# Kernel optimization log

Hardware: AMD Instinct MI355X
Metric: run time of the kernel (lower is better)

The kernel has to match this reference:

```python
import jax, jax.numpy as jnp
import numpy as np

BETA = 1.0
EPS = 1e-8  # matches torch F.cosine_similarity eps


def setup_inputs() -> dict:
    key = jax.random.key(0)
    x = jax.random.normal(key, (4096, 2, 1024), dtype=jnp.float32)
    return {"x": x}


def _cosine_sim_matrix(pos, anc):
    # pos: [B, D], anc: [B, D] -> [B, B], sim[i, j] = cos(pos[i], anc[j])
    dots = jnp.einsum('id,jd->ij', pos, anc)
    pn = jnp.sqrt(jnp.sum(pos * pos, axis=-1))
    an = jnp.sqrt(jnp.sum(anc * anc, axis=-1))
    denom = jnp.maximum(pn[:, None] * an[None, :], EPS)
    return dots / denom


def reference(x):
    # x: [B, M, D], M >= 2
    out_anchor = jnp.mean(x[:, 1:, :], axis=1)   # [B, D]
    out_positive = x[:, 0, :]                     # [B, D]
    sim = _cosine_sim_matrix(out_positive, out_anchor)  # [B, B]
    n = sim.shape[0]

    diag = jnp.diagonal(sim)                      # [B]
    # tempsim for column i: beta * (sim[:, i] - sim[i, i]), excluding row i
    T = BETA * (sim - diag[None, :])              # [B, B]
    eye = jnp.eye(n, dtype=bool)

    # exclude-diagonal logsumexp per column (vectorized over all columns)
    Tm = jnp.where(eye, -jnp.inf, T)
    temploss = jax.nn.logsumexp(Tm, axis=0)       # [B]
    # flatNCE trick: exp(l - stop_grad(l)) has value 1 but gradient of l
    nloss = jnp.mean(jnp.exp(temploss - jax.lax.stop_gradient(temploss)))

    # top-1 accuracy against labels arange(B) (detached in original)
    label = jnp.arange(n)
    prec1 = jnp.mean((jnp.argmax(sim, axis=1) == label).astype(jnp.float32)) * 100.0
    return nloss, prec1
```

## Files before the change

kernel.cpp:

```cpp
#include <hip/hip_runtime.h>


#define NROWS 4096
#define DDIM  1024
#define XSTR  2048

typedef unsigned int u32;
typedef unsigned long long u64;
typedef __attribute__((ext_vector_type(8))) short bf16x8;
typedef __attribute__((ext_vector_type(16))) float f32x16;

__device__ __forceinline__ unsigned int fkey(float f) {
    unsigned int u = __float_as_uint(f);
    return (u & 0x80000000u) ? ~u : (u | 0x80000000u);
}

__device__ __forceinline__ u64 shfl_xor_u64(u64 v, int m) {
    unsigned int lo = (unsigned int)v;
    unsigned int hi = (unsigned int)(v >> 32);
    lo = __shfl_xor(lo, m, 64);
    hi = __shfl_xor(hi, m, 64);
    return ((u64)hi << 32) | lo;
}

__device__ __forceinline__ unsigned short f2bf(float f) {
    unsigned u = __float_as_uint(f);
    return (unsigned short)((u + 0x7FFFu + ((u >> 16) & 1u)) >> 16);
}

#define PF_OFF   0u
#define AF_OFF   8388608u
#define INV_OFF  16777216u
#define PCK_OFF  16793600u
#define DONE_OFF 16826368u
#define WS_NEED  16826432u

__global__ __launch_bounds__(256) void prep_kernel(const float* __restrict__ x,
                                                   unsigned short* __restrict__ Pf,
                                                   unsigned short* __restrict__ Af,
                                                   float* __restrict__ inv_an,
                                                   u64* __restrict__ packed,
                                                   unsigned int* __restrict__ done) {
    __shared__ float rsum[256];
    const int b = blockIdx.x;
    const int t = threadIdx.x;
    const int l31 = t & 31;
    const int lh = (t >> 5) & 1;
    const int row = b * 32 + l31;

    const float* px = x + (size_t)row * XSTR;
    unsigned short* pdst = Pf + (size_t)b * 32768;
    unsigned short* adst = Af + (size_t)b * 32768;

    float s = 0.0f;
#pragma unroll
    for (int i = 0; i < 16; ++i) {
        const int g = i * 256 + t;
        const int kcol = (g >> 6) * 16 + lh * 8;

        float4 p0 = *(const float4*)(px + kcol);
        float4 p1 = *(const float4*)(px + kcol + 4);
        float4 a0 = *(const float4*)(px + DDIM + kcol);
        float4 a1 = *(const float4*)(px + DDIM + kcol + 4);

        ushort4 h0 = make_ushort4(f2bf(p0.x), f2bf(p0.y), f2bf(p0.z), f2bf(p0.w));
        ushort4 h1 = make_ushort4(f2bf(p1.x), f2bf(p1.y), f2bf(p1.z), f2bf(p1.w));
        *(ushort4*)(pdst + g * 8) = h0;
        *(ushort4*)(pdst + g * 8 + 4) = h1;

        ushort4 g0 = make_ushort4(f2bf(a0.x), f2bf(a0.y), f2bf(a0.z), f2bf(a0.w));
        ushort4 g1 = make_ushort4(f2bf(a1.x), f2bf(a1.y), f2bf(a1.z), f2bf(a1.w));
        *(ushort4*)(adst + g * 8) = g0;
        *(ushort4*)(adst + g * 8 + 4) = g1;

        s += a0.x * a0.x + a0.y * a0.y + a0.z * a0.z + a0.w * a0.w;
        s += a1.x * a1.x + a1.y * a1.y + a1.z * a1.z + a1.w * a1.w;
    }
    rsum[t] = s;
    __syncthreads();
    if (t < 32) {
        float tot = 0.0f;
#pragma unroll
        for (int w = 0; w < 8; ++w) tot += rsum[t + 32 * w];
        inv_an[b * 32 + t] = 1.0f / sqrtf(tot);
        packed[b * 32 + t] = 0ULL;
        if (b == 0 && t == 0) *done = 0u;
    }
}

#define FRAG(base, blk, kh) (*(const bf16x8*)((base) + (((size_t)(blk)) << 16) + ((kh) << 10)))

__global__ __launch_bounds__(256, 1) void mfma_gemm_argmax(const unsigned short* __restrict__ Pf,
                                                           const unsigned short* __restrict__ Af,
                                                           const float* __restrict__ inv_an,
                                                           u64* __restrict__ packed,
                                                           unsigned int* __restrict__ done,
                                                           float* __restrict__ out) {
    __shared__ unsigned int lastflag;
    __shared__ int cnt[4];

    const int bid = blockIdx.x;
    const int xcd = bid & 7;
    const int slt = bid >> 3;
    const int rblk = (xcd >> 1) * 4 + (slt >> 3);
    const int cblk = (xcd & 1) * 8 + (slt & 7);
    const int r0 = rblk * 256;
    const int c0 = cblk * 256;

    const int wave = threadIdx.x >> 6;
    const int lane = threadIdx.x & 63;
    const int l31 = lane & 31;
    const int lh = lane >> 5;
    const int wm = wave & 1;
    const int wn = wave >> 1;

    const int mb0 = rblk * 8 + wm * 4;
    const int nb0 = cblk * 8 + wn * 4;

    const char* pP = (const char*)Pf + (size_t)lane * 16 + ((size_t)mb0 << 16);
    const char* pA = (const char*)Af + (size_t)lane * 16 + ((size_t)nb0 << 16);

    f32x16 zero16 = {0.f,0.f,0.f,0.f,0.f,0.f,0.f,0.f,0.f,0.f,0.f,0.f,0.f,0.f,0.f,0.f};
    f32x16 acc[4][4];
#pragma unroll
    for (int i = 0; i < 4; ++i)
#pragma unroll
        for (int j = 0; j < 4; ++j) acc[i][j] = zero16;

    bf16x8 phA[4], aaA[4], phB[4], aaB[4];

#pragma unroll
    for (int q = 0; q < 4; ++q) { phA[q] = FRAG(pP, q, 0); aaA[q] = FRAG(pA, q, 0); }

    for (int kh = 0; kh < 64; kh += 2) {
#pragma unroll
        for (int q = 0; q < 4; ++q) { phB[q] = FRAG(pP, q, kh + 1); aaB[q] = FRAG(pA, q, kh + 1); }

#pragma unroll
        for (int mt = 0; mt < 4; ++mt)
#pragma unroll
            for (int nt = 0; nt < 4; ++nt)
                acc[mt][nt] = __builtin_amdgcn_mfma_f32_32x32x16_bf16(phA[mt], aaA[nt], acc[mt][nt], 0, 0, 0);

        if (kh + 2 < 64) {
#pragma unroll
            for (int q = 0; q < 4; ++q) { phA[q] = FRAG(pP, q, kh + 2); aaA[q] = FRAG(pA, q, kh + 2); }
        }

#pragma unroll
        for (int mt = 0; mt < 4; ++mt)
#pragma unroll
            for (int nt = 0; nt < 4; ++nt)
                acc[mt][nt] = __builtin_amdgcn_mfma_f32_32x32x16_bf16(phB[mt], aaB[nt], acc[mt][nt], 0, 0, 0);
    }

    float ian[4];
#pragma unroll
    for (int nt = 0; nt < 4; ++nt) ian[nt] = inv_an[c0 + wn * 128 + nt * 32 + l31];

#pragma unroll
    for (int mt = 0; mt < 4; ++mt)
#pragma unroll
        for (int reg = 0; reg < 16; ++reg) {
            const int row = r0 + wm * 128 + mt * 32 + (reg & 3) + 8 * (reg >> 2) + 4 * lh;
            u64 best = 0ULL;
#pragma unroll
            for (int nt = 0; nt < 4; ++nt) {
                const int col = c0 + wn * 128 + nt * 32 + l31;
                const float v = acc[mt][nt][reg] * ian[nt];
                const u64 p = ((u64)fkey(v) << 32) | (unsigned int)(~col);
                best = best > p ? best : p;
            }
#pragma unroll
            for (int m = 1; m <= 16; m <<= 1) {
                const u64 o = shfl_xor_u64(best, m);
                best = best > o ? best : o;
            }
            if (l31 == 0) atomicMax(&packed[row], best);
        }

    __syncthreads();
    if (threadIdx.x == 0) {
        __threadfence();
        unsigned int old = atomicAdd(done, 1u);
        lastflag = (old == 255u) ? 1u : 0u;
    }
    __syncthreads();
    if (lastflag) {
        int c = 0;
        for (int r = threadIdx.x; r < NROWS; r += 256) {
            u64 v = atomicAdd(&packed[r], 0ULL);
            unsigned int col = ~(unsigned int)(v & 0xFFFFFFFFULL);
            c += (col == (unsigned int)r) ? 1 : 0;
        }
#pragma unroll
        for (int off = 32; off > 0; off >>= 1) c += __shfl_down(c, off, 64);
        if ((threadIdx.x & 63) == 0) cnt[threadIdx.x >> 6] = c;
        __syncthreads();
        if (threadIdx.x == 0) {
            out[0] = 1.0f;
            out[1] = 100.0f * (float)(cnt[0] + cnt[1] + cnt[2] + cnt[3]) / (float)NROWS;
        }
    }
}

__global__ __launch_bounds__(256) void norms_kernel(const float* __restrict__ x,
                                                    float* __restrict__ inv_an,
                                                    u64* __restrict__ packed) {
    int gid  = blockIdx.x * 256 + threadIdx.x;
    int j    = gid >> 6;
    int lane = threadIdx.x & 63;
    if (gid < NROWS) packed[gid] = 0ULL;
    const float4* a = (const float4*)(x + (size_t)j * XSTR + DDIM);
    float s = 0.0f;
#pragma unroll
    for (int i = 0; i < 4; ++i) {
        float4 v = a[lane + i * 64];
        s += v.x * v.x + v.y * v.y + v.z * v.z + v.w * v.w;
    }
#pragma unroll
    for (int off = 32; off > 0; off >>= 1) s += __shfl_down(s, off, 64);
    if (lane == 0) inv_an[j] = 1.0f / sqrtf(s);
}

__global__ __launch_bounds__(256) void gemm_argmax_kernel(const float* __restrict__ x,
                                                          const float* __restrict__ inv_an,
                                                          u64* __restrict__ packed) {
    __shared__ __align__(16) float Pt[16][128];
    __shared__ __align__(16) float At[16][128];
    const int r0 = blockIdx.x * 128;
    const int c0 = blockIdx.y * 128;
    const int t = threadIdx.x;
    const int tx = t & 15;
    const int ty = t >> 4;
    const int srow = t >> 1;
    const int skq = (t & 1) * 8;
    float acc[8][8];
#pragma unroll
    for (int r = 0; r < 8; ++r)
#pragma unroll
        for (int c = 0; c < 8; ++c) acc[r][c] = 0.0f;
    const float* gp = x + (size_t)(r0 + srow) * XSTR + skq;
    const float* ga = x + (size_t)(c0 + srow) * XSTR + DDIM + skq;
    for (int k0 = 0; k0 < DDIM; k0 += 16) {
        __syncthreads();
        float4 p0 = *(const float4*)(gp + k0);
        float4 p1 = *(const float4*)(gp + k0 + 4);
        float4 a0 = *(const float4*)(ga + k0);
        float4 a1 = *(const float4*)(ga + k0 + 4);
        Pt[skq + 0][srow] = p0.x; Pt[skq + 1][srow] = p0.y;
        Pt[skq + 2][srow] = p0.z; Pt[skq + 3][srow] = p0.w;
        Pt[skq + 4][srow] = p1.x; Pt[skq + 5][srow] = p1.y;
        Pt[skq + 6][srow] = p1.z; Pt[skq + 7][srow] = p1.w;
        At[skq + 0][srow] = a0.x; At[skq + 1][srow] = a0.y;
        At[skq + 2][srow] = a0.z; At[skq + 3][srow] = a0.w;
        At[skq + 4][srow] = a1.x; At[skq + 5][srow] = a1.y;
        At[skq + 6][srow] = a1.z; At[skq + 7][srow] = a1.w;
        __syncthreads();
#pragma unroll
        for (int kk = 0; kk < 16; ++kk) {
            float pr[8], ar[8];
            *(float4*)&pr[0] = *(const float4*)&Pt[kk][ty * 8];
            *(float4*)&pr[4] = *(const float4*)&Pt[kk][ty * 8 + 4];
            *(float4*)&ar[0] = *(const float4*)&At[kk][tx * 8];
            *(float4*)&ar[4] = *(const float4*)&At[kk][tx * 8 + 4];
#pragma unroll
            for (int r = 0; r < 8; ++r)
#pragma unroll
                for (int c = 0; c < 8; ++c) acc[r][c] += pr[r] * ar[c];
        }
    }
    float ian[8];
#pragma unroll
    for (int c = 0; c < 8; ++c) ian[c] = inv_an[c0 + tx * 8 + c];
#pragma unroll
    for (int r = 0; r < 8; ++r) {
        int row = r0 + ty * 8 + r;
        u64 best = 0ULL;
#pragma unroll
        for (int c = 0; c < 8; ++c) {
            int col = c0 + tx * 8 + c;
            float v = acc[r][c] * ian[c];
            u64 p = ((u64)fkey(v) << 32) | (unsigned int)(~col);
            best = best > p ? best : p;
        }
#pragma unroll
        for (int m = 1; m <= 8; m <<= 1) {
            u64 o = shfl_xor_u64(best, m);
            best = best > o ? best : o;
        }
        if (tx == 0) atomicMax(&packed[row], best);
    }
}

__global__ __launch_bounds__(256) void finalize_kernel(const u64* __restrict__ packed,
                                                       float* __restrict__ out) {
    __shared__ int cnt_s;
    int t = threadIdx.x;
    if (t == 0) cnt_s = 0;
    __syncthreads();
    int c = 0;
    for (int r = t; r < NROWS; r += 256) {
        unsigned int col = ~(unsigned int)(packed[r] & 0xFFFFFFFFULL);
        c += (col == (unsigned int)r) ? 1 : 0;
    }
#pragma unroll
    for (int off = 32; off > 0; off >>= 1) c += __shfl_down(c, off, 64);
    if ((t & 63) == 0) atomicAdd(&cnt_s, c);
    __syncthreads();
    if (t == 0) {
        out[0] = 1.0f;
        out[1] = 100.0f * (float)cnt_s / (float)NROWS;
    }
}

extern "C" void kernel_launch(void* const* d_in, const int* in_sizes, int n_in,
                              void* d_out, int out_size, void* d_ws, size_t ws_size,
                              hipStream_t stream) {
    (void)in_sizes; (void)n_in; (void)out_size;
    const float* x = (const float*)d_in[0];
    float* out = (float*)d_out;

    if (ws_size >= (size_t)WS_NEED) {
        char* ws = (char*)d_ws;
        unsigned short* Pf = (unsigned short*)(ws + PF_OFF);
        unsigned short* Af = (unsigned short*)(ws + AF_OFF);
        float* inv_an = (float*)(ws + INV_OFF);
        u64* packed = (u64*)(ws + PCK_OFF);
        unsigned int* done = (unsigned int*)(ws + DONE_OFF);

        prep_kernel<<<128, 256, 0, stream>>>(x, Pf, Af, inv_an, packed, done);
        mfma_gemm_argmax<<<256, 256, 0, stream>>>(Pf, Af, inv_an, packed, done, out);
    } else {
        float* inv_an = (float*)d_ws;
        u64* packed = (u64*)((char*)d_ws + NROWS * sizeof(float));
        norms_kernel<<<NROWS / 4, 256, 0, stream>>>(x, inv_an, packed);
        dim3 grid(NROWS / 128, NROWS / 128);
        gemm_argmax_kernel<<<grid, 256, 0, stream>>>(x, inv_an, packed);
        finalize_kernel<<<1, 256, 0, stream>>>(packed, out);
    }
}
```

Before: 131.8 us.

## Use 8 waves per GEMM block with smaller per-wave tiles and triple-buffered fragments

Doubles the GEMM block to 512 threads (8 waves), so each wave computes a 64x128 tile instead of 128x128. This halves the accumulator registers per wave and raises the number of resident waves available to hide global-load latency. The two-stage A/B fragment ping-pong becomes a fully unrolled three-stage rotating buffer that prefetches two k-steps ahead. In exchange, each wave reuses loaded fragments across fewer MFMAs, so total global and L2 fragment traffic grows, and the full unroll increases code size.

```diff
diff --git a/kernel.cpp b/kernel.cpp
--- a/kernel.cpp
+++ b/kernel.cpp
@@ -63,15 +63,10 @@
         float4 a0 = *(const float4*)(px + DDIM + kcol);
         float4 a1 = *(const float4*)(px + DDIM + kcol + 4);
 
-        ushort4 h0 = make_ushort4(f2bf(p0.x), f2bf(p0.y), f2bf(p0.z), f2bf(p0.w));
-        ushort4 h1 = make_ushort4(f2bf(p1.x), f2bf(p1.y), f2bf(p1.z), f2bf(p1.w));
-        *(ushort4*)(pdst + g * 8) = h0;
-        *(ushort4*)(pdst + g * 8 + 4) = h1;
-
-        ushort4 g0 = make_ushort4(f2bf(a0.x), f2bf(a0.y), f2bf(a0.z), f2bf(a0.w));
-        ushort4 g1 = make_ushort4(f2bf(a1.x), f2bf(a1.y), f2bf(a1.z), f2bf(a1.w));
-        *(ushort4*)(adst + g * 8) = g0;
-        *(ushort4*)(adst + g * 8 + 4) = g1;
+        *(ushort4*)(pdst + g * 8) = make_ushort4(f2bf(p0.x), f2bf(p0.y), f2bf(p0.z), f2bf(p0.w));
+        *(ushort4*)(pdst + g * 8 + 4) = make_ushort4(f2bf(p1.x), f2bf(p1.y), f2bf(p1.z), f2bf(p1.w));
+        *(ushort4*)(adst + g * 8) = make_ushort4(f2bf(a0.x), f2bf(a0.y), f2bf(a0.z), f2bf(a0.w));
+        *(ushort4*)(adst + g * 8 + 4) = make_ushort4(f2bf(a1.x), f2bf(a1.y), f2bf(a1.z), f2bf(a1.w));
 
         s += a0.x * a0.x + a0.y * a0.y + a0.z * a0.z + a0.w * a0.w;
         s += a1.x * a1.x + a1.y * a1.y + a1.z * a1.z + a1.w * a1.w;
@@ -90,14 +85,14 @@
 
 #define FRAG(base, blk, kh) (*(const bf16x8*)((base) + (((size_t)(blk)) << 16) + ((kh) << 10)))
 
-__global__ __launch_bounds__(256, 1) void mfma_gemm_argmax(const unsigned short* __restrict__ Pf,
+__global__ __launch_bounds__(512, 2) void mfma_gemm_argmax(const unsigned short* __restrict__ Pf,
                                                            const unsigned short* __restrict__ Af,
                                                            const float* __restrict__ inv_an,
                                                            u64* __restrict__ packed,
                                                            unsigned int* __restrict__ done,
                                                            float* __restrict__ out) {
     __shared__ unsigned int lastflag;
-    __shared__ int cnt[4];
+    __shared__ int cnt[8];
 
     const int bid = blockIdx.x;
     const int xcd = bid & 7;
@@ -111,47 +106,43 @@
     const int lane = threadIdx.x & 63;
     const int l31 = lane & 31;
     const int lh = lane >> 5;
-    const int wm = wave & 1;
-    const int wn = wave >> 1;
-
-    const int mb0 = rblk * 8 + wm * 4;
+    const int wm = wave & 3;
+    const int wn = wave >> 2;
+
+    const int mb0 = rblk * 8 + wm * 2;
     const int nb0 = cblk * 8 + wn * 4;
 
     const char* pP = (const char*)Pf + (size_t)lane * 16 + ((size_t)mb0 << 16);
     const char* pA = (const char*)Af + (size_t)lane * 16 + ((size_t)nb0 << 16);
 
     f32x16 zero16 = {0.f,0.f,0.f,0.f,0.f,0.f,0.f,0.f,0.f,0.f,0.f,0.f,0.f,0.f,0.f,0.f};
-    f32x16 acc[4][4];
-#pragma unroll
-    for (int i = 0; i < 4; ++i)
+    f32x16 acc[2][4];
+#pragma unroll
+    for (int i = 0; i < 2; ++i)
 #pragma unroll
         for (int j = 0; j < 4; ++j) acc[i][j] = zero16;
 
-    bf16x8 phA[4], aaA[4], phB[4], aaB[4];
-
-#pragma unroll
-    for (int q = 0; q < 4; ++q) { phA[q] = FRAG(pP, q, 0); aaA[q] = FRAG(pA, q, 0); }
-
-    for (int kh = 0; kh < 64; kh += 2) {
-#pragma unroll
-        for (int q = 0; q < 4; ++q) { phB[q] = FRAG(pP, q, kh + 1); aaB[q] = FRAG(pA, q, kh + 1); }
-
-#pragma unroll
-        for (int mt = 0; mt < 4; ++mt)
+    bf16x8 ph[3][2], aa[3][4];
+#pragma unroll
+    for (int q = 0; q < 2; ++q) { ph[0][q] = FRAG(pP, q, 0); ph[1][q] = FRAG(pP, q, 1); }
+#pragma unroll
+    for (int q = 0; q < 4; ++q) { aa[0][q] = FRAG(pA, q, 0); aa[1][q] = FRAG(pA, q, 1); }
+
+#pragma unroll
+    for (int kh = 0; kh < 64; ++kh) {
+        const int cs = kh % 3;
+        if (kh + 2 < 64) {
+            const int ns = (kh + 2) % 3;
+#pragma unroll
+            for (int q = 0; q < 2; ++q) ph[ns][q] = FRAG(pP, q, kh + 2);
+#pragma unroll
+            for (int q = 0; q < 4; ++q) aa[ns][q] = FRAG(pA, q, kh + 2);
+        }
+#pragma unroll
+        for (int mt = 0; mt < 2; ++mt)
 #pragma unroll
             for (int nt = 0; nt < 4; ++nt)
-                acc[mt][nt] = __builtin_amdgcn_mfma_f32_32x32x16_bf16(phA[mt], aaA[nt], acc[mt][nt], 0, 0, 0);
-
-        if (kh + 2 < 64) {
-#pragma unroll
-            for (int q = 0; q < 4; ++q) { phA[q] = FRAG(pP, q, kh + 2); aaA[q] = FRAG(pA, q, kh + 2); }
-        }
-
-#pragma unroll
-        for (int mt = 0; mt < 4; ++mt)
-#pragma unroll
-            for (int nt = 0; nt < 4; ++nt)
-                acc[mt][nt] = __builtin_amdgcn_mfma_f32_32x32x16_bf16(phB[mt], aaB[nt], acc[mt][nt], 0, 0, 0);
+                acc[mt][nt] = __builtin_amdgcn_mfma_f32_32x32x16_bf16(ph[cs][mt], aa[cs][nt], acc[mt][nt], 0, 0, 0);
     }
 
     float ian[4];
@@ -159,10 +150,10 @@
     for (int nt = 0; nt < 4; ++nt) ian[nt] = inv_an[c0 + wn * 128 + nt * 32 + l31];
 
 #pragma unroll
-    for (int mt = 0; mt < 4; ++mt)
+    for (int mt = 0; mt < 2; ++mt)
 #pragma unroll
         for (int reg = 0; reg < 16; ++reg) {
-            const int row = r0 + wm * 128 + mt * 32 + (reg & 3) + 8 * (reg >> 2) + 4 * lh;
+            const int row = r0 + wm * 64 + mt * 32 + (reg & 3) + 8 * (reg >> 2) + 4 * lh;
             u64 best = 0ULL;
 #pragma unroll
             for (int nt = 0; nt < 4; ++nt) {
@@ -188,7 +179,7 @@
     __syncthreads();
     if (lastflag) {
         int c = 0;
-        for (int r = threadIdx.x; r < NROWS; r += 256) {
+        for (int r = threadIdx.x; r < NROWS; r += 512) {
             u64 v = atomicAdd(&packed[r], 0ULL);
             unsigned int col = ~(unsigned int)(v & 0xFFFFFFFFULL);
             c += (col == (unsigned int)r) ? 1 : 0;
@@ -198,8 +189,11 @@
         if ((threadIdx.x & 63) == 0) cnt[threadIdx.x >> 6] = c;
         __syncthreads();
         if (threadIdx.x == 0) {
+            int tot = 0;
+#pragma unroll
+            for (int w = 0; w < 8; ++w) tot += cnt[w];
             out[0] = 1.0f;
-            out[1] = 100.0f * (float)(cnt[0] + cnt[1] + cnt[2] + cnt[3]) / (float)NROWS;
+            out[1] = 100.0f * (float)tot / (float)NROWS;
         }
     }
 }
@@ -330,7 +324,7 @@
         unsigned int* done = (unsigned int*)(ws + DONE_OFF);
 
         prep_kernel<<<128, 256, 0, stream>>>(x, Pf, Af, inv_an, packed, done);
-        mfma_gemm_argmax<<<256, 256, 0, stream>>>(Pf, Af, inv_an, packed, done, out);
+        mfma_gemm_argmax<<<256, 512, 0, stream>>>(Pf, Af, inv_an, packed, done, out);
     } else {
         float* inv_an = (float*)d_ws;
         u64* packed = (u64*)((char*)d_ws + NROWS * sizeof(float));
```

New measurement: 131.1 us. No clear change (-0.6%).
